# Kernel tuning notes

Measured on AMD Instinct MI355X. Metric: run time of the kernel, lower is better.

## Reference

```python
import jax, jax.numpy as jnp
import numpy as np

LS, BS, N_HID, N_PART, T, D_IN, M = 2, 16, 256, 512, 16, 64, 1
MID = N_PART // 2


def setup_inputs() -> dict:
    key = jax.random.key(0)
    ks = jax.random.split(key, 12)
    s = 0.1
    inp = {}
    inp["x"] = jax.random.normal(ks[0], (BS, T, D_IN), jnp.float32)
    inp["y"] = jax.random.normal(ks[1], (BS,), jnp.float32)
    inp["particles"] = jax.random.normal(ks[2], (LS, BS, N_HID, N_PART), jnp.float32)
    inp["weights"] = jnp.full((BS, N_PART), 1.0 / N_PART, jnp.float32)
    inp["q"] = jnp.asarray(1.0, jnp.float32)
    inp["e"] = jnp.asarray(0.1, jnp.float32)
    inp["r"] = jnp.asarray(0.5, jnp.float32)
    inp["Wih0"] = jax.random.normal(ks[3], (4 * N_HID, D_IN), jnp.float32) * s
    inp["Whh0"] = jax.random.normal(ks[4], (4 * N_HID, N_HID), jnp.float32) * s
    inp["b0"] = jnp.zeros((4 * N_HID,), jnp.float32)
    inp["Wih1"] = jax.random.normal(ks[5], (4 * N_HID, N_HID), jnp.float32) * s
    inp["Whh1"] = jax.random.normal(ks[6], (4 * N_HID, N_HID), jnp.float32) * s
    inp["b1"] = jnp.zeros((4 * N_HID,), jnp.float32)
    inp["Wh"] = jax.random.normal(ks[7], (M, N_HID), jnp.float32) * s
    inp["bh"] = jnp.zeros((M,), jnp.float32)
    inp["eps_h"] = jax.random.normal(ks[8], (MID, LS, BS, N_HID), jnp.float32)
    inp["eps_c"] = jax.random.normal(ks[9], (MID, LS, BS, N_HID), jnp.float32)
    u = jax.random.uniform(ks[10], (BS, 2, MID), jnp.float32, minval=1e-6, maxval=1.0)
    inp["gumbel"] = -jnp.log(-jnp.log(u))  # Gumbel noise for multinomial resampling
    return inp


def _lstm(x, h0, c0, Wih0, Whh0, b0, Wih1, Whh1, b1, q2, e2, eps_h, eps_c):
    # x: [bs,T,d]; h0,c0: [ls,bs,n]. Two-layer LSTM, noise added to final states.
    xs = jnp.swapaxes(x, 0, 1)  # [T,bs,d]

    def make_step(Wih, Whh, b):
        def step(carry, xt):
            h, c = carry
            g = xt @ Wih.T + h @ Whh.T + b
            i, f, gg, o = jnp.split(g, 4, axis=-1)
            c2 = jax.nn.sigmoid(f) * c + jax.nn.sigmoid(i) * jnp.tanh(gg)
            h2 = jax.nn.sigmoid(o) * jnp.tanh(c2)
            return (h2, c2), h2
        return step

    (hA, cA), out0 = jax.lax.scan(make_step(Wih0, Whh0, b0), (h0[0], c0[0]), xs)
    (hB, cB), out1 = jax.lax.scan(make_step(Wih1, Whh1, b1), (h0[1], c0[1]), out0)
    hT = jnp.stack([hA, hB]) + jnp.sqrt(q2) * eps_h
    cT = jnp.stack([cA, cB]) + jnp.sqrt(e2) * eps_c
    return jnp.swapaxes(out1, 0, 1), hT, cT


def _obs(u_last, Wh, bh):  # u_last: [bs,n,N] -> [bs,m,N]
    return jnp.einsum('mn,bnN->bmN', Wh, u_last) + bh[None, :, None]


def _estimate(Y, w, r):
    # Y: [bs,m,N], w: [bs,N]
    w_sum = jnp.sum(w, -1)
    W_mu = jnp.einsum('bmN,bN->bm', Y, w) / w_sum[:, None]
    cen = Y - W_mu[:, :, None]
    cov = jnp.einsum('bmN,bkN->bmk', cen, cen) / (Y.shape[-1] - 1)
    cov = cov + jnp.eye(Y.shape[1], dtype=Y.dtype) * (r * r)
    return W_mu, cov


def _inv_logdet(sig):
    m = sig.shape[-1]
    sig = sig + 1e-6 * jnp.eye(m, dtype=sig.dtype)
    L = jnp.linalg.cholesky(sig)
    inv_sig = jnp.linalg.inv(jnp.swapaxes(L, -2, -1)) @ jnp.linalg.inv(L)
    logdet = jnp.linalg.slogdet(sig)[1]
    return inv_sig, logdet


def reference(x, y, particles, weights, q, e, r, Wih0, Whh0, b0, Wih1, Whh1, b1, Wh, bh, eps_h, eps_c, gumbel):
    q2, e2 = q * q, e * e  # noise is squared before the transition (TransitionF)
    # ---- forecast_PF: particle i is h, particle i+MID is c ----
    h_parts = jnp.moveaxis(particles[..., :MID], -1, 0)  # [MID,ls,bs,n]
    c_parts = jnp.moveaxis(particles[..., MID:], -1, 0)
    step_fn = jax.vmap(lambda h0, c0, eh, ec: _lstm(x, h0, c0, Wih0, Whh0, b0, Wih1, Whh1, b1, q2, e2, eh, ec)[1:])
    hN, cN = step_fn(h_parts, c_parts, eps_h, eps_c)
    pr = jnp.moveaxis(jnp.concatenate([hN, cN], 0), 0, -1)  # [ls,bs,n,N]

    # ---- torch_PF weight update ----
    w = jnp.log(weights)
    Y = _obs(pr[-1], Wh, bh)  # [bs,m,N]
    W_mu_e, sig_e = _estimate(Y, w, r)  # NOTE: original passes LOG weights here (faithful)
    inv_sig, logdet = _inv_logdet(sig_e)
    w_sum = jnp.sum(w, -1)
    Wmu2 = Y * w[:, None, :] / w_sum[:, None, None]  # elementwise, as in w_likelihood
    innov = y[:, None, None] - Wmu2  # [bs,m,N]
    quad = jnp.einsum('bmN,bmk,bkN->bN', innov, inv_sig, innov)
    new_w = w + (-0.5 * logdet[:, None] - 0.5 * quad)
    # original: new_w -= log(sum(exp(new_w))) where python-sum reduces dim 0 -> [N]
    new_w = new_w - jnp.log(jnp.sum(jnp.exp(new_w), axis=0))[None, :]
    new_w = jnp.exp(new_w)

    # ---- per-batch, per-half soft resampling when neff < N/4 ----
    def resample_half(p, wh, g):  # p [ls,n,MID], wh [MID], g [MID]
        neff = 1.0 / jnp.sum(wh * wh)
        do = neff < (N_PART / 4.0)
        soft = 0.5 * wh + 0.5 / MID
        idx = jnp.argsort(-(jnp.log(soft) + g))  # weighted sample w/o replacement (Gumbel top-k)
        p_r = p[:, :, idx]
        lw = jnp.log(wh / soft)
        w_r = jnp.exp(lw - jax.nn.logsumexp(lw))
        return jnp.where(do, p_r, p), jnp.where(do, w_r, wh)

    def per_batch(p_b, w_b, g_b):  # p_b [ls,n,N], w_b [N], g_b [2,MID]
        p1, w1 = resample_half(p_b[:, :, :MID], w_b[:MID], g_b[0])
        p2, w2 = resample_half(p_b[:, :, MID:], w_b[MID:], g_b[1])
        return jnp.concatenate([p1, p2], -1), jnp.concatenate([w1, w2], 0)

    pf, wf = jax.vmap(per_batch, in_axes=(1, 0, 0), out_axes=(1, 0))(pr, new_w, gumbel)

    # ---- train=True branch: estimate / likelihood / NIS on filtered ensemble ----
    Yf = _obs(pf[-1], Wh, bh)
    W_mu, sig = _estimate(Yf, wf, r)
    inv_s, ld = _inv_logdet(sig)
    inn = y[:, None] - W_mu  # [bs,m]
    qf = jnp.einsum('bm,bmk,bk->b', inn, inv_s, inn)
    l = jnp.sum(-0.5 * ld - 0.5 * qf)
    nis = jnp.mean(qf)
    return W_mu, sig, pf, wf, l, nis
```

## Files before the change

### kernel.cpp

```cpp
#include <hip/hip_runtime.h>
#include <hip/hip_bf16.h>
#include <math.h>

#define LSN 2
#define BSN 16
#define NH 256
#define NP 512
#define MIDP 256
#define TTN 16
#define DIN 64
#define NCH 4096
#define GW 1024
#define PRS 268
#define BUFSZ 36864

typedef _Float16 f16;
typedef _Float16 f16x8 __attribute__((ext_vector_type(8)));
typedef float f32x4 __attribute__((ext_vector_type(4)));

__device__ __forceinline__ float fsig(float x){ return 1.0f/(1.0f+expf(-x)); }

__device__ __forceinline__ float brsum512(float v, float* red){
  int tid = threadIdx.x;
  red[tid]=v; __syncthreads();
  for (int s=256; s>0; s>>=1){ if (tid<s) red[tid]+=red[tid+s]; __syncthreads(); }
  float r = red[0]; __syncthreads(); return r;
}
__device__ __forceinline__ float brsum(float v, float* red){
  int tid = threadIdx.x;
  red[tid]=v; __syncthreads();
  for (int s=128; s>0; s>>=1){ if (tid<s) red[tid]+=red[tid+s]; __syncthreads(); }
  float r = red[0]; __syncthreads(); return r;
}

__device__ __forceinline__ int gsrow(int jp){
  return ((jp>>5)&3)*NH + (jp>>7)*32 + (jp&31);
}

__global__ __launch_bounds__(256) void k_prep_all(
    const float* __restrict__ Whh0, const float* __restrict__ Wih1,
    const float* __restrict__ Whh1, const float* __restrict__ b1,
    const float* __restrict__ x, const float* __restrict__ Wih0,
    const float* __restrict__ b0, const float* __restrict__ part,
    f16* __restrict__ W0i, f16* __restrict__ W1c, float* __restrict__ b1i,
    float* __restrict__ xW0,
    f16* __restrict__ h0, f16* __restrict__ h1,
    float* __restrict__ c0, float* __restrict__ c1)
{
  __shared__ float lh[64][65];
  __shared__ float lcv[64][65];
  int bid = blockIdx.x;
  int tid = threadIdx.x;
  if (bid < 1024){
    int jp = bid; int srow = gsrow(jp); int t = tid;
    W0i[(size_t)jp*NH + t]        = (f16)Whh0[(size_t)srow*NH + t];
    W1c[(size_t)jp*512 + t]       = (f16)Wih1[(size_t)srow*NH + t];
    W1c[(size_t)jp*512 + 256 + t] = (f16)Whh1[(size_t)srow*NH + t];
    if (t==0) b1i[jp] = b1[srow];
  } else if (bid < 1280){
    int row = bid - 1024;
    float* xr = lh[0];
    if (tid < DIN) xr[tid] = x[(size_t)row*DIN + tid];
    __syncthreads();
    int n = tid;
    for (int q=0;q<4;++q){
      int wrow = q*NH + n;
      float acc = b0[wrow];
      #pragma unroll 8
      for (int d=0; d<DIN; ++d) acc += xr[d] * Wih0[(size_t)wrow*DIN + d];
      int jhat = (n>>5)*128 + q*32 + (n&31);
      xW0[(size_t)row*GW + jhat] = acc;
    }
  } else {
    int idx = bid - 1280;
    int xb = idx & 15, b = (idx>>4)&15, l = idx>>8;
    int i0 = (xb >> 2)*64, n0 = (xb & 3)*64;
    #pragma unroll
    for (int rep=0; rep<16; ++rep){
      int nn = rep*4 + (tid>>6);
      int ii = tid & 63;
      size_t rowb = ((size_t)(l*BSN + b)*NH + n0 + nn)*NP;
      lh[nn][ii]  = part[rowb + i0 + ii];
      lcv[nn][ii] = part[rowb + MIDP + i0 + ii];
    }
    __syncthreads();
    f16* h = l ? h1 : h0;
    float* c = l ? c1 : c0;
    #pragma unroll
    for (int rep=0; rep<16; ++rep){
      int ii = rep*4 + (tid>>6);
      int nn = tid & 63;
      size_t chain = (size_t)b*256 + i0 + ii;
      h[chain*NH + n0 + nn] = (f16)lh[nn][ii];
      c[chain*NH + n0 + nn] = lcv[nn][ii];
    }
  }
}

struct StepCfg {
  const f16* A1; const f16* A2;
  float* C; f16* Hout;
  int layer; int t; int is_last;
};

__global__ __launch_bounds__(256, 4) void k_step2(
    StepCfg cfgA, StepCfg cfgB,
    const f16* __restrict__ W0i, const f16* __restrict__ W1c,
    const float* __restrict__ xw0, const float* __restrict__ b1i,
    float* __restrict__ pr, const float* __restrict__ eps_h, const float* __restrict__ eps_c,
    const float* __restrict__ qp, const float* __restrict__ ep)
{
  __shared__ __align__(16) char smem[BUFSZ];

  const int bid = blockIdx.x;
  const int xcd = bid & 7, jj = bid >> 3;
  const int mloc = jj & 3, y = (jj >> 2) & 7, z = (jj >> 5) & 1;
  const int mt = xcd*4 + mloc;
  const int m0 = mt * 128;

  const StepCfg cfg = z ? cfgB : cfgA;
  const int layer  = cfg.layer;
  const int Kt     = layer ? 512 : 256;
  const int nslice = layer ? 8 : 4;
  const f16* W     = layer ? W1c : W0i;

  const int tid = threadIdx.x;
  const int lane = tid & 63, wid = tid >> 6;
  const int lr = lane >> 4, lc = lane & 15;
  const int wm = wid * 32;
  const int bb = mt >> 1;

  f16* Asm = (f16*)smem;
  f16* Bsm = Asm + 128*72;
  float* prstage = (float*)smem;

  float cold[2][2][4];
  #pragma unroll
  for (int mi=0; mi<2; ++mi)
    #pragma unroll
    for (int mh=0; mh<2; ++mh)
      #pragma unroll
      for (int r=0; r<4; ++r)
        cold[mi][mh][r] = cfg.C[(size_t)(m0 + wm + mi*16 + lr*4 + r)*NH + y*32 + mh*16 + lc];

  f32x4 acc[2][8];
  #pragma unroll
  for (int mi=0;mi<2;++mi)
    #pragma unroll
    for (int ni=0;ni<8;++ni) acc[mi][ni] = (f32x4){0.f,0.f,0.f,0.f};

  const int srow = tid >> 1, sseg = (tid & 1)*32;
  for (int ks=0; ks<nslice; ++ks){
    __syncthreads();
    const f16* Ab; int ka;
    if (layer==1 && ks>=4){ Ab = cfg.A2; ka = (ks-4)*64; } else { Ab = cfg.A1; ka = ks*64; }
    {
      const float4* sa = (const float4*)(Ab + (size_t)(m0+srow)*NH + ka + sseg);
      float4* da = (float4*)(Asm + srow*72 + sseg);
      da[0]=sa[0]; da[1]=sa[1]; da[2]=sa[2]; da[3]=sa[3];
      const float4* sb = (const float4*)(W + (size_t)(y*128+srow)*Kt + (size_t)ks*64 + sseg);
      float4* db = (float4*)(Bsm + srow*72 + sseg);
      db[0]=sb[0]; db[1]=sb[1]; db[2]=sb[2]; db[3]=sb[3];
    }
    __syncthreads();
    #pragma unroll
    for (int k2=0;k2<2;++k2){
      const int koff = k2*32 + lr*8;
      f16x8 a0 = *(const f16x8*)(Asm + (wm +  0 + lc)*72 + koff);
      f16x8 a1 = *(const f16x8*)(Asm + (wm + 16 + lc)*72 + koff);
      f16x8 b[8];
      #pragma unroll
      for (int ni=0;ni<8;++ni) b[ni] = *(const f16x8*)(Bsm + (ni*16 + lc)*72 + koff);
      #pragma unroll
      for (int ni=0;ni<8;++ni){
        acc[0][ni] = __builtin_amdgcn_mfma_f32_16x16x32_f16(a0, b[ni], acc[0][ni], 0,0,0);
        acc[1][ni] = __builtin_amdgcn_mfma_f32_16x16x32_f16(a1, b[ni], acc[1][ni], 0,0,0);
      }
    }
  }

  float addv[4][2];
  {
    const float* ar = (layer==0) ? (xw0 + (size_t)(bb*TTN + cfg.t)*GW + y*128)
                                 : (b1i + y*128);
    #pragma unroll
    for (int q=0;q<4;++q)
      #pragma unroll
      for (int mh=0;mh<2;++mh)
        addv[q][mh] = ar[q*32 + mh*16 + lc];
  }

  float sq=0.f, se=0.f;
  if (cfg.is_last){
    sq = sqrtf(qp[0]*qp[0]); se = sqrtf(ep[0]*ep[0]);
    __syncthreads();
  }

  #pragma unroll
  for (int mi=0;mi<2;++mi)
   #pragma unroll
   for (int mh=0;mh<2;++mh)
    #pragma unroll
    for (int r=0;r<4;++r){
      float gi = acc[mi][mh+0][r] + addv[0][mh];
      float gf = acc[mi][mh+2][r] + addv[1][mh];
      float gg = acc[mi][mh+4][r] + addv[2][mh];
      float go = acc[mi][mh+6][r] + addv[3][mh];
      float c2 = fsig(gf)*cold[mi][mh][r] + fsig(gi)*tanhf(gg);
      float h2 = fsig(go)*tanhf(c2);
      int ml = wm + mi*16 + lr*4 + r;
      int chain = m0 + ml;
      int nglob = y*32 + mh*16 + lc;
      cfg.Hout[(size_t)chain*NH + nglob] = (f16)h2;
      if (!cfg.is_last){
        cfg.C[(size_t)chain*NH + nglob] = c2;
      } else {
        int ip = (mt & 1)*128 + ml;
        size_t eidx = ((size_t)(ip*LSN + layer)*BSN + bb)*NH + nglob;
        int nl = mh*16 + lc;
        prstage[nl*PRS + ml]       = h2 + sq*eps_h[eidx];
        prstage[nl*PRS + 128 + ml] = c2 + se*eps_c[eidx];
      }
    }

  if (cfg.is_last){
    __syncthreads();
    #pragma unroll
    for (int s=0;s<8;++s){
      int u = s*256 + tid;
      int nl = u >> 6, within = u & 63;
      int half = within >> 5, q4 = within & 31;
      size_t rowp = (size_t)(layer*BSN + bb)*NH + y*32 + nl;
      float4 v = *(const float4*)(prstage + nl*PRS + half*128 + q4*4);
      *(float4*)(pr + rowp*NP + half*MIDP + (mt & 1)*128 + q4*4) = v;
    }
  }
}

__global__ void k_obs_stats(const float* __restrict__ pr, const float* __restrict__ Wh,
                            const float* __restrict__ bh, const float* __restrict__ wts,
                            const float* __restrict__ yv, const float* __restrict__ rp,
                            float* __restrict__ Y, float* __restrict__ pre){
  int b = blockIdx.x; int N = threadIdx.x;
  __shared__ float red[512];
  float acc = bh[0];
  #pragma unroll 4
  for (int n=0;n<NH;++n) acc += Wh[n] * pr[((size_t)(BSN + b)*NH + n)*NP + N];
  Y[(size_t)b*NP + N] = acc;
  float lw = logf(wts[b*NP+N]);
  float SW = brsum512(lw, red);
  float SY = brsum512(acc*lw, red);
  float mu = SY/SW;
  float cen = acc-mu;
  float SC = brsum512(cen*cen, red);
  float sig = SC/511.0f + rp[0]*rp[0];
  float a = sig+1e-6f, inv = 1.0f/a, ld = logf(a);
  float i0 = yv[b] - acc*lw/SW;
  pre[b*NP+N] = lw - 0.5f*ld - 0.5f*inv*i0*i0;
}

__global__ void k_resample(const float* __restrict__ pre, const float* __restrict__ gum,
                           const float* __restrict__ Y,
                           float* __restrict__ wf, int* __restrict__ idxb, int* __restrict__ dofl,
                           float* __restrict__ Yf, float* __restrict__ out){
  int b = blockIdx.x >> 1, hf = blockIdx.x & 1, j = threadIdx.x;
  __shared__ float red[256]; __shared__ float key[256]; __shared__ int sidx[256];
  int N = hf*256 + j;
  float s=0.f;
  for(int b2=0;b2<BSN;b2++) s += expf(pre[b2*NP+N]);
  float ls = logf(s);
  float wh = expf(pre[b*NP+N] - ls);
  red[j] = wh*wh; __syncthreads();
  for (int s2i=128;s2i>0;s2i>>=1){ if(j<s2i) red[j]+=red[j+s2i]; __syncthreads(); }
  float s2 = red[0]; __syncthreads();
  int doit = (1.0f/s2) < (float)(NP)/4.0f;
  float soft = 0.5f*wh + (0.5f/(float)MIDP);
  float kk = logf(soft) + gum[(b*2+hf)*256 + j];
  key[j] = kk; __syncthreads();
  int rank = 0;
  for (int m=0;m<256;++m){ float km = key[m]; rank += (km > kk) || (km == kk && m < j); }
  sidx[rank] = j; __syncthreads();
  idxb[(b*2+hf)*256 + j] = sidx[j];
  int dcol = doit ? hf*256 + sidx[j] : N;
  Yf[b*NP + N] = Y[b*NP + dcol];
  float lw = logf(wh/soft);
  red[j] = lw; __syncthreads();
  for (int s2i=128;s2i>0;s2i>>=1){ if(j<s2i) red[j] = fmaxf(red[j],red[j+s2i]); __syncthreads(); }
  float mx = red[0]; __syncthreads();
  red[j] = expf(lw-mx); __syncthreads();
  for (int s2i=128;s2i>0;s2i>>=1){ if(j<s2i) red[j]+=red[j+s2i]; __syncthreads(); }
  float lse = mx + logf(red[0]);
  float wr = expf(lw - lse);
  float wv = doit ? wr : wh;
  wf[b*NP + N] = wv;
  out[4194336 + b*NP + N] = wv;
  if (j==0) dofl[b*2+hf] = doit;
}

__global__ void k_pfg(const float* __restrict__ pr, const int* __restrict__ idxb,
                      const int* __restrict__ dofl, float* __restrict__ out){
  __shared__ int dcol[512];
  int blk = blockIdx.x;
  int q = blk & 3, lb = blk >> 2;
  int b = lb & 15;
  int tid = threadIdx.x;
  #pragma unroll
  for (int hf=0; hf<2; ++hf){
    int N = hf*256 + tid;
    dcol[N] = dofl[b*2+hf] ? hf*256 + idxb[(b*2+hf)*256 + tid] : N;
  }
  __syncthreads();
  int d0 = dcol[tid], d1 = dcol[tid+256];
  size_t rowbase = (size_t)lb*NH + q*64;
  for (int rr=0; rr<64; ++rr){
    size_t row = rowbase + rr;
    const float* src = pr + row*NP;
    float* dst = out + 32 + row*NP;
    dst[tid]     = src[d0];
    dst[tid+256] = src[d1];
  }
}

__global__ void k_final_est(const float* __restrict__ Yf, const float* __restrict__ wf,
                            const float* __restrict__ yv, const float* __restrict__ rp,
                            float* __restrict__ qf, float* __restrict__ ldb,
                            float* __restrict__ out){
  int b = blockIdx.x, tid = threadIdx.x;
  __shared__ float red[256];
  float w0 = wf[b*NP+tid], w1 = wf[b*NP+256+tid];
  float y0 = Yf[b*NP+tid], y1 = Yf[b*NP+256+tid];
  float SW = brsum(w0+w1, red);
  float SY = brsum(y0*w0+y1*w1, red);
  float mu = SY/SW;
  float c0=y0-mu, c1=y1-mu;
  float SC = brsum(c0*c0+c1*c1, red);
  float sig = SC/511.0f + rp[0]*rp[0];
  if (tid==0){
    float a = sig + 1e-6f; float inv = 1.0f/a; float ld = logf(a);
    float inn = yv[b]-mu; float q = inn*inn*inv;
    qf[b]=q; ldb[b]=ld;
    out[b]      = mu;
    out[16 + b] = sig;
  }
}

__global__ void k_final_scalar(const float* __restrict__ qf, const float* __restrict__ ldb,
                               float* __restrict__ out){
  if (threadIdx.x==0){
    float l=0.f, nq=0.f;
    for(int b=0;b<BSN;b++){ l += -0.5f*ldb[b]-0.5f*qf[b]; nq += qf[b]; }
    out[4202528] = l;
    out[4202529] = nq/16.0f;
  }
}

extern "C" void kernel_launch(void* const* d_in, const int* in_sizes, int n_in,
                              void* d_out, int out_size, void* d_ws, size_t ws_size,
                              hipStream_t stream) {
  const float* x      = (const float*)d_in[0];
  const float* yv     = (const float*)d_in[1];
  const float* part   = (const float*)d_in[2];
  const float* wts    = (const float*)d_in[3];
  const float* qp     = (const float*)d_in[4];
  const float* ep     = (const float*)d_in[5];
  const float* rp     = (const float*)d_in[6];
  const float* Wih0   = (const float*)d_in[7];
  const float* Whh0   = (const float*)d_in[8];
  const float* b0     = (const float*)d_in[9];
  const float* Wih1   = (const float*)d_in[10];
  const float* Whh1   = (const float*)d_in[11];
  const float* b1     = (const float*)d_in[12];
  const float* Wh     = (const float*)d_in[13];
  const float* bh     = (const float*)d_in[14];
  const float* eps_h  = (const float*)d_in[15];
  const float* eps_c  = (const float*)d_in[16];
  const float* gum    = (const float*)d_in[17];
  float* out = (float*)d_out;

  char* p = (char*)d_ws;
  f16*   W0i  = (f16*)p;  p += (size_t)GW*NH*2;
  f16*   W1c  = (f16*)p;  p += (size_t)GW*512*2;
  float* b1i  = (float*)p; p += (size_t)GW*4;
  float* xW0  = (float*)p; p += (size_t)256*GW*4;
  f16*   h0A  = (f16*)p;  p += (size_t)NCH*NH*2;
  f16*   h0B  = (f16*)p;  p += (size_t)NCH*NH*2;
  f16*   h1A  = (f16*)p;  p += (size_t)NCH*NH*2;
  f16*   h1B  = (f16*)p;  p += (size_t)NCH*NH*2;
  float* c0   = (float*)p; p += (size_t)NCH*NH*4;
  float* c1   = (float*)p; p += (size_t)NCH*NH*4;
  float* pr   = (float*)p; p += (size_t)LSN*BSN*NH*NP*4;
  float* Yb   = (float*)p; p += 32768;
  float* pre  = (float*)p; p += 32768;
  float* wf   = (float*)p; p += 32768;
  float* Yf   = (float*)p; p += 32768;
  int*   idxb = (int*)p;   p += 32768;
  int*   dofl = (int*)p;   p += 128;
  float* qf   = (float*)p; p += 64;
  float* ldb  = (float*)p; p += 64;

  k_prep_all<<<1792, 256, 0, stream>>>(Whh0, Wih1, Whh1, b1, x, Wih0, b0, part,
                                       W0i, W1c, b1i, xW0, h0A, h1A, c0, c1);

  {
    StepCfg s0{h0A, nullptr, c0, h0B, 0, 0, 0};
    k_step2<<<256, 256, 0, stream>>>(s0, s0, W0i, W1c, xW0, b1i,
        pr, eps_h, eps_c, qp, ep);
  }
  f16 *h0cur=h0B, *h0nxt=h0A, *h1cur=h1A, *h1nxt=h1B;
  for (int t=0; t<15; ++t){
    StepCfg ca{h0cur, nullptr, c0, h0nxt, 0, t+1, (t+1==15) ? 1 : 0};
    StepCfg cb{h0cur, h1cur,   c1, h1nxt, 1, t,   0};
    k_step2<<<512, 256, 0, stream>>>(ca, cb, W0i, W1c, xW0, b1i,
        pr, eps_h, eps_c, qp, ep);
    f16* tmp = h0cur; h0cur = h0nxt; h0nxt = tmp;
    tmp = h1cur; h1cur = h1nxt; h1nxt = tmp;
  }
  {
    StepCfg fin{h0cur, h1cur, c1, h1nxt, 1, 15, 1};
    k_step2<<<256, 256, 0, stream>>>(fin, fin, W0i, W1c, xW0, b1i,
        pr, eps_h, eps_c, qp, ep);
  }

  k_obs_stats <<<16, 512, 0, stream>>>(pr, Wh, bh, wts, yv, rp, Yb, pre);
  k_resample  <<<32, 256, 0, stream>>>(pre, gum, Yb, wf, idxb, dofl, Yf, out);
  k_pfg       <<<128, 256, 0, stream>>>(pr, idxb, dofl, out);
  k_final_est <<<16, 256, 0, stream>>>(Yf, wf, yv, rp, qf, ldb, out);
  k_final_scalar<<<1, 64, 0, stream>>>(qf, ldb, out);
}
```

Before: 437.7 us.

## Fuse all LSTM timesteps into one persistent kernel keeping state on-chip

Replaces the 17 per-timestep step kernel launches with a single persistent kernel of 128 blocks. Each block owns 32 chains for all 16 timesteps of both layers, keeping h in double-buffered shared memory and c in registers. Weights are read straight from global/L2 into registers instead of being staged through LDS. This removes launch overhead and the global round-trips of h/c state between steps. The cost is lower parallelism (128 blocks, one per CU), repeated weight reads from cache each step, and serial per-block work with no inter-block overlap.

```diff
diff --git a/kernel.cpp b/kernel.cpp
--- a/kernel.cpp
+++ b/kernel.cpp
@@ -11,8 +11,6 @@
 #define DIN 64
 #define NCH 4096
 #define GW 1024
-#define PRS 268
-#define BUFSZ 36864
 
 typedef _Float16 f16;
 typedef _Float16 f16x8 __attribute__((ext_vector_type(8)));
@@ -97,143 +95,178 @@
   }
 }
 
-struct StepCfg {
-  const f16* A1; const f16* A2;
-  float* C; f16* Hout;
-  int layer; int t; int is_last;
-};
-
-__global__ __launch_bounds__(256, 4) void k_step2(
-    StepCfg cfgA, StepCfg cfgB,
+__global__ __launch_bounds__(256, 1) void k_lstm_all(
     const f16* __restrict__ W0i, const f16* __restrict__ W1c,
     const float* __restrict__ xw0, const float* __restrict__ b1i,
+    const f16* __restrict__ h0A, const f16* __restrict__ h1A,
+    const float* __restrict__ c0g, const float* __restrict__ c1g,
     float* __restrict__ pr, const float* __restrict__ eps_h, const float* __restrict__ eps_c,
     const float* __restrict__ qp, const float* __restrict__ ep)
 {
-  __shared__ __align__(16) char smem[BUFSZ];
+  __shared__ __align__(16) f16 h0l[2][4][32*72];
+  __shared__ __align__(16) f16 h1l[2][4][32*72];
 
   const int bid = blockIdx.x;
-  const int xcd = bid & 7, jj = bid >> 3;
-  const int mloc = jj & 3, y = (jj >> 2) & 7, z = (jj >> 5) & 1;
-  const int mt = xcd*4 + mloc;
-  const int m0 = mt * 128;
-
-  const StepCfg cfg = z ? cfgB : cfgA;
-  const int layer  = cfg.layer;
-  const int Kt     = layer ? 512 : 256;
-  const int nslice = layer ? 8 : 4;
-  const f16* W     = layer ? W1c : W0i;
-
   const int tid = threadIdx.x;
   const int lane = tid & 63, wid = tid >> 6;
   const int lr = lane >> 4, lc = lane & 15;
-  const int wm = wid * 32;
-  const int bb = mt >> 1;
-
-  f16* Asm = (f16*)smem;
-  f16* Bsm = Asm + 128*72;
-  float* prstage = (float*)smem;
-
-  float cold[2][2][4];
+  const int bb = bid >> 3;
+  const int i0 = (bid & 7) * 32;
+  const int chain0 = bid * 32;
+
+  {
+    int rr = tid >> 3, seg = (tid & 7) * 32;
+    int slice = seg >> 6, within = seg & 63;
+    const float4* s0 = (const float4*)(h0A + (size_t)(chain0 + rr)*NH + seg);
+    float4* d0 = (float4*)(&h0l[0][slice][rr*72 + within]);
+    d0[0]=s0[0]; d0[1]=s0[1]; d0[2]=s0[2]; d0[3]=s0[3];
+    const float4* s1 = (const float4*)(h1A + (size_t)(chain0 + rr)*NH + seg);
+    float4* d1 = (float4*)(&h1l[0][slice][rr*72 + within]);
+    d1[0]=s1[0]; d1[1]=s1[1]; d1[2]=s1[2]; d1[3]=s1[3];
+  }
+
+  float c0s[2][2][2][4], c1s[2][2][2][4];
   #pragma unroll
-  for (int mi=0; mi<2; ++mi)
+  for (int yy=0; yy<2; ++yy){
+    int y = wid*2 + yy;
     #pragma unroll
-    for (int mh=0; mh<2; ++mh)
-      #pragma unroll
-      for (int r=0; r<4; ++r)
-        cold[mi][mh][r] = cfg.C[(size_t)(m0 + wm + mi*16 + lr*4 + r)*NH + y*32 + mh*16 + lc];
-
-  f32x4 acc[2][8];
-  #pragma unroll
-  for (int mi=0;mi<2;++mi)
+    for (int mi=0; mi<2; ++mi)
+      #pragma unroll
+      for (int mh=0; mh<2; ++mh)
+        #pragma unroll
+        for (int r=0; r<4; ++r){
+          int row = mi*16 + lr*4 + r;
+          int n = y*32 + mh*16 + lc;
+          c0s[yy][mi][mh][r] = c0g[(size_t)(chain0+row)*NH + n];
+          c1s[yy][mi][mh][r] = c1g[(size_t)(chain0+row)*NH + n];
+        }
+  }
+  const float sq = sqrtf(qp[0]*qp[0]);
+  const float se = sqrtf(ep[0]*ep[0]);
+
+  __syncthreads();
+
+  int cur0 = 0, cur1 = 0;
+  for (int t = 0; t < 16; ++t){
+    const int last = (t == 15);
     #pragma unroll
-    for (int ni=0;ni<8;++ni) acc[mi][ni] = (f32x4){0.f,0.f,0.f,0.f};
-
-  const int srow = tid >> 1, sseg = (tid & 1)*32;
-  for (int ks=0; ks<nslice; ++ks){
-    __syncthreads();
-    const f16* Ab; int ka;
-    if (layer==1 && ks>=4){ Ab = cfg.A2; ka = (ks-4)*64; } else { Ab = cfg.A1; ka = ks*64; }
-    {
-      const float4* sa = (const float4*)(Ab + (size_t)(m0+srow)*NH + ka + sseg);
-      float4* da = (float4*)(Asm + srow*72 + sseg);
-      da[0]=sa[0]; da[1]=sa[1]; da[2]=sa[2]; da[3]=sa[3];
-      const float4* sb = (const float4*)(W + (size_t)(y*128+srow)*Kt + (size_t)ks*64 + sseg);
-      float4* db = (float4*)(Bsm + srow*72 + sseg);
-      db[0]=sb[0]; db[1]=sb[1]; db[2]=sb[2]; db[3]=sb[3];
+    for (int yy=0; yy<2; ++yy){
+      const int y = wid*2 + yy;
+      f32x4 acc[2][8];
+      #pragma unroll
+      for (int mi=0;mi<2;++mi)
+        #pragma unroll
+        for (int ni=0;ni<8;++ni) acc[mi][ni] = (f32x4){0.f,0.f,0.f,0.f};
+      for (int ks=0; ks<4; ++ks){
+        #pragma unroll
+        for (int k2=0;k2<2;++k2){
+          const int koff = k2*32 + lr*8;
+          f16x8 a0 = *(const f16x8*)(&h0l[cur0][ks][( 0 + lc)*72 + koff]);
+          f16x8 a1 = *(const f16x8*)(&h0l[cur0][ks][(16 + lc)*72 + koff]);
+          f16x8 b[8];
+          #pragma unroll
+          for (int ni=0;ni<8;++ni)
+            b[ni] = *(const f16x8*)(W0i + (size_t)(y*128 + ni*16 + lc)*NH + ks*64 + koff);
+          #pragma unroll
+          for (int ni=0;ni<8;++ni){
+            acc[0][ni] = __builtin_amdgcn_mfma_f32_16x16x32_f16(a0, b[ni], acc[0][ni], 0,0,0);
+            acc[1][ni] = __builtin_amdgcn_mfma_f32_16x16x32_f16(a1, b[ni], acc[1][ni], 0,0,0);
+          }
+        }
+      }
+      const float* ar = xw0 + (size_t)(bb*TTN + t)*GW + y*128;
+      float addv[4][2];
+      #pragma unroll
+      for (int q=0;q<4;++q)
+        #pragma unroll
+        for (int mh=0;mh<2;++mh)
+          addv[q][mh] = ar[q*32 + mh*16 + lc];
+      #pragma unroll
+      for (int mi=0;mi<2;++mi)
+       #pragma unroll
+       for (int mh=0;mh<2;++mh)
+        #pragma unroll
+        for (int r=0;r<4;++r){
+          float gi = acc[mi][mh+0][r] + addv[0][mh];
+          float gf = acc[mi][mh+2][r] + addv[1][mh];
+          float gg = acc[mi][mh+4][r] + addv[2][mh];
+          float go = acc[mi][mh+6][r] + addv[3][mh];
+          float c2 = fsig(gf)*c0s[yy][mi][mh][r] + fsig(gi)*tanhf(gg);
+          float h2 = fsig(go)*tanhf(c2);
+          c0s[yy][mi][mh][r] = c2;
+          int row = mi*16 + lr*4 + r;
+          int n = y*32 + mh*16 + lc;
+          h0l[cur0^1][n>>6][row*72 + (n&63)] = (f16)h2;
+          if (last){
+            int ip = i0 + row;
+            size_t eidx = ((size_t)(ip*LSN + 0)*BSN + bb)*NH + n;
+            size_t rowp = (size_t)(0*BSN + bb)*NH + n;
+            pr[rowp*NP + ip]        = h2 + sq*eps_h[eidx];
+            pr[rowp*NP + MIDP + ip] = c2 + se*eps_c[eidx];
+          }
+        }
     }
     __syncthreads();
     #pragma unroll
-    for (int k2=0;k2<2;++k2){
-      const int koff = k2*32 + lr*8;
-      f16x8 a0 = *(const f16x8*)(Asm + (wm +  0 + lc)*72 + koff);
-      f16x8 a1 = *(const f16x8*)(Asm + (wm + 16 + lc)*72 + koff);
-      f16x8 b[8];
-      #pragma unroll
-      for (int ni=0;ni<8;++ni) b[ni] = *(const f16x8*)(Bsm + (ni*16 + lc)*72 + koff);
-      #pragma unroll
-      for (int ni=0;ni<8;++ni){
-        acc[0][ni] = __builtin_amdgcn_mfma_f32_16x16x32_f16(a0, b[ni], acc[0][ni], 0,0,0);
-        acc[1][ni] = __builtin_amdgcn_mfma_f32_16x16x32_f16(a1, b[ni], acc[1][ni], 0,0,0);
+    for (int yy=0; yy<2; ++yy){
+      const int y = wid*2 + yy;
+      f32x4 acc[2][8];
+      #pragma unroll
+      for (int mi=0;mi<2;++mi)
+        #pragma unroll
+        for (int ni=0;ni<8;++ni) acc[mi][ni] = (f32x4){0.f,0.f,0.f,0.f};
+      for (int ks=0; ks<8; ++ks){
+        const f16* Asl = (ks < 4) ? &h0l[cur0^1][ks][0] : &h1l[cur1][ks-4][0];
+        #pragma unroll
+        for (int k2=0;k2<2;++k2){
+          const int koff = k2*32 + lr*8;
+          f16x8 a0 = *(const f16x8*)(Asl + ( 0 + lc)*72 + koff);
+          f16x8 a1 = *(const f16x8*)(Asl + (16 + lc)*72 + koff);
+          f16x8 b[8];
+          #pragma unroll
+          for (int ni=0;ni<8;++ni)
+            b[ni] = *(const f16x8*)(W1c + (size_t)(y*128 + ni*16 + lc)*512 + ks*64 + koff);
+          #pragma unroll
+          for (int ni=0;ni<8;++ni){
+            acc[0][ni] = __builtin_amdgcn_mfma_f32_16x16x32_f16(a0, b[ni], acc[0][ni], 0,0,0);
+            acc[1][ni] = __builtin_amdgcn_mfma_f32_16x16x32_f16(a1, b[ni], acc[1][ni], 0,0,0);
+          }
+        }
       }
+      const float* ar = b1i + y*128;
+      float addv[4][2];
+      #pragma unroll
+      for (int q=0;q<4;++q)
+        #pragma unroll
+        for (int mh=0;mh<2;++mh)
+          addv[q][mh] = ar[q*32 + mh*16 + lc];
+      #pragma unroll
+      for (int mi=0;mi<2;++mi)
+       #pragma unroll
+       for (int mh=0;mh<2;++mh)
+        #pragma unroll
+        for (int r=0;r<4;++r){
+          float gi = acc[mi][mh+0][r] + addv[0][mh];
+          float gf = acc[mi][mh+2][r] + addv[1][mh];
+          float gg = acc[mi][mh+4][r] + addv[2][mh];
+          float go = acc[mi][mh+6][r] + addv[3][mh];
+          float c2 = fsig(gf)*c1s[yy][mi][mh][r] + fsig(gi)*tanhf(gg);
+          float h2 = fsig(go)*tanhf(c2);
+          c1s[yy][mi][mh][r] = c2;
+          int row = mi*16 + lr*4 + r;
+          int n = y*32 + mh*16 + lc;
+          h1l[cur1^1][n>>6][row*72 + (n&63)] = (f16)h2;
+          if (last){
+            int ip = i0 + row;
+            size_t eidx = ((size_t)(ip*LSN + 1)*BSN + bb)*NH + n;
+            size_t rowp = (size_t)(1*BSN + bb)*NH + n;
+            pr[rowp*NP + ip]        = h2 + sq*eps_h[eidx];
+            pr[rowp*NP + MIDP + ip] = c2 + se*eps_c[eidx];
+          }
+        }
     }
-  }
-
-  float addv[4][2];
-  {
-    const float* ar = (layer==0) ? (xw0 + (size_t)(bb*TTN + cfg.t)*GW + y*128)
-                                 : (b1i + y*128);
-    #pragma unroll
-    for (int q=0;q<4;++q)
-      #pragma unroll
-      for (int mh=0;mh<2;++mh)
-        addv[q][mh] = ar[q*32 + mh*16 + lc];
-  }
-
-  float sq=0.f, se=0.f;
-  if (cfg.is_last){
-    sq = sqrtf(qp[0]*qp[0]); se = sqrtf(ep[0]*ep[0]);
     __syncthreads();
-  }
-
-  #pragma unroll
-  for (int mi=0;mi<2;++mi)
-   #pragma unroll
-   for (int mh=0;mh<2;++mh)
-    #pragma unroll
-    for (int r=0;r<4;++r){
-      float gi = acc[mi][mh+0][r] + addv[0][mh];
-      float gf = acc[mi][mh+2][r] + addv[1][mh];
-      float gg = acc[mi][mh+4][r] + addv[2][mh];
-      float go = acc[mi][mh+6][r] + addv[3][mh];
-      float c2 = fsig(gf)*cold[mi][mh][r] + fsig(gi)*tanhf(gg);
-      float h2 = fsig(go)*tanhf(c2);
-      int ml = wm + mi*16 + lr*4 + r;
-      int chain = m0 + ml;
-      int nglob = y*32 + mh*16 + lc;
-      cfg.Hout[(size_t)chain*NH + nglob] = (f16)h2;
-      if (!cfg.is_last){
-        cfg.C[(size_t)chain*NH + nglob] = c2;
-      } else {
-        int ip = (mt & 1)*128 + ml;
-        size_t eidx = ((size_t)(ip*LSN + layer)*BSN + bb)*NH + nglob;
-        int nl = mh*16 + lc;
-        prstage[nl*PRS + ml]       = h2 + sq*eps_h[eidx];
-        prstage[nl*PRS + 128 + ml] = c2 + se*eps_c[eidx];
-      }
-    }
-
-  if (cfg.is_last){
-    __syncthreads();
-    #pragma unroll
-    for (int s=0;s<8;++s){
-      int u = s*256 + tid;
-      int nl = u >> 6, within = u & 63;
-      int half = within >> 5, q4 = within & 31;
-      size_t rowp = (size_t)(layer*BSN + bb)*NH + y*32 + nl;
-      float4 v = *(const float4*)(prstage + nl*PRS + half*128 + q4*4);
-      *(float4*)(pr + rowp*NP + half*MIDP + (mt & 1)*128 + q4*4) = v;
-    }
+    cur0 ^= 1; cur1 ^= 1;
   }
 }
 
@@ -397,29 +430,13 @@
   int*   dofl = (int*)p;   p += 128;
   float* qf   = (float*)p; p += 64;
   float* ldb  = (float*)p; p += 64;
+  (void)h0B; (void)h1B;
 
   k_prep_all<<<1792, 256, 0, stream>>>(Whh0, Wih1, Whh1, b1, x, Wih0, b0, part,
                                        W0i, W1c, b1i, xW0, h0A, h1A, c0, c1);
 
-  {
-    StepCfg s0{h0A, nullptr, c0, h0B, 0, 0, 0};
-    k_step2<<<256, 256, 0, stream>>>(s0, s0, W0i, W1c, xW0, b1i,
-        pr, eps_h, eps_c, qp, ep);
-  }
-  f16 *h0cur=h0B, *h0nxt=h0A, *h1cur=h1A, *h1nxt=h1B;
-  for (int t=0; t<15; ++t){
-    StepCfg ca{h0cur, nullptr, c0, h0nxt, 0, t+1, (t+1==15) ? 1 : 0};
-    StepCfg cb{h0cur, h1cur,   c1, h1nxt, 1, t,   0};
-    k_step2<<<512, 256, 0, stream>>>(ca, cb, W0i, W1c, xW0, b1i,
-        pr, eps_h, eps_c, qp, ep);
-    f16* tmp = h0cur; h0cur = h0nxt; h0nxt = tmp;
-    tmp = h1cur; h1cur = h1nxt; h1nxt = tmp;
-  }
-  {
-    StepCfg fin{h0cur, h1cur, c1, h1nxt, 1, 15, 1};
-    k_step2<<<256, 256, 0, stream>>>(fin, fin, W0i, W1c, xW0, b1i,
-        pr, eps_h, eps_c, qp, ep);
-  }
+  k_lstm_all<<<128, 256, 0, stream>>>(W0i, W1c, xW0, b1i, h0A, h1A, c0, c1,
+                                      pr, eps_h, eps_c, qp, ep);
 
   k_obs_stats <<<16, 512, 0, stream>>>(pr, Wh, bh, wts, yv, rp, Yb, pre);
   k_resample  <<<32, 256, 0, stream>>>(pre, gum, Yb, wf, idxb, dofl, Yf, out);
```

Result: slower. 1.212 ms (+176.9%).
